# Optimization experiments

Hardware: AMD Instinct MI355X
Metric: run time of the kernel (lower is better)

Reference implementation:

```python
import jax, jax.numpy as jnp
import numpy as np

EPS = 1e-6
BN_EPS = 1e-5
K = 20

def vn_linear(x, W):
    # x: (B, Cin, 3, ...), W: (Cout, Cin)
    return jnp.einsum('oc,bc...->bo...', W, x)

def vn_batchnorm(x, gamma, beta):
    # x: (B, C, 3, ...). BN (training-mode batch stats) over per-channel vector norms.
    n = jnp.linalg.norm(x, axis=2) + EPS               # (B, C, ...)
    red = (0,) + tuple(range(2, n.ndim))
    mu = n.mean(red, keepdims=True)
    var = ((n - mu) ** 2).mean(red, keepdims=True)     # biased var, as BatchNorm uses
    sh = (1, -1) + (1,) * (n.ndim - 2)
    nbn = (n - mu) / jnp.sqrt(var + BN_EPS) * gamma.reshape(sh) + beta.reshape(sh)
    return x / n[:, :, None] * nbn[:, :, None]

def vn_leaky(x, Wf, Wd, gamma, beta, ns):
    # VNLinearLeakyReLU: linear -> VN batchnorm -> direction-gated leaky relu
    p = vn_batchnorm(vn_linear(x, Wf), gamma, beta)
    d = vn_linear(x, Wd)
    dot = jnp.sum(p * d, axis=2, keepdims=True)
    dsq = jnp.sum(d * d, axis=2, keepdims=True) + EPS
    neg = p - (dot / dsq) * d
    return ns * p + (1.0 - ns) * jnp.where(dot >= 0, p, neg)

def graph_feature_cross(x, k):
    # x: (B, N, 3) -> edge features (B, 3, 3, N, k): [nbr - x, x, nbr x x]
    sq = jnp.sum(x * x, axis=-1)                        # (B, N)
    d2 = sq[:, :, None] + sq[:, None, :] - 2.0 * jnp.einsum('bnd,bmd->bnm', x, x)
    idx = jax.lax.top_k(-d2, k)[1]                      # (B, N, k) nearest incl. self
    nbr = jax.vmap(lambda pts, ind: pts[ind])(x, idx)   # (B, N, k, 3)
    c = jnp.broadcast_to(x[:, :, None, :], nbr.shape)
    cr = jnp.cross(nbr, c)
    feat = jnp.stack([nbr - c, c, cr], axis=3)          # (B, N, k, 3ch, 3)
    return jnp.transpose(feat, (0, 3, 4, 1, 2))         # (B, 3, 3, N, k)


def setup_inputs() -> dict:
    key = jax.random.key(0)
    ks = iter(jax.random.split(key, 40))
    def W(shape):
        return jax.random.normal(next(ks), shape, jnp.float32) * 0.05
    d = {'x': jax.random.normal(next(ks), (2, 2048, 3), jnp.float32)}
    d.update(
        Wf_pos=W((21, 3)), Wd_pos=W((21, 3)), g_pos=jnp.ones(21), be_pos=jnp.zeros(21),
        Wf1=W((21, 21)), Wd1=W((21, 21)), g1=jnp.ones(21), be1=jnp.zeros(21),
        Wf2=W((42, 21)), Wd2=W((42, 21)), g2=jnp.ones(42), be2=jnp.zeros(42),
        W3=W((170, 42)), g3=jnp.ones(170), be3=jnp.zeros(170),
        Ws1f=W((170, 340)), Ws1d=W((170, 340)), gs1=jnp.ones(170), bs1=jnp.zeros(170),
        Ws2f=W((85, 170)), Ws2d=W((85, 170)), gs2=jnp.ones(85), bs2=jnp.zeros(85),
        Wstd=W((3, 85)),
        Wt1=W((1020, 1020)), Wt2=W((1020, 1020)), Wt3=W((14450, 1020)), bt3=jnp.zeros(14450),
    )
    return d


def reference(x, Wf_pos, Wd_pos, g_pos, be_pos, Wf1, Wd1, g1, be1, Wf2, Wd2, g2, be2,
              W3, g3, be3, Ws1f, Ws1d, gs1, bs1, Ws2f, Ws2d, gs2, bs2, Wstd,
              Wt1, Wt2, Wt3, bt3):
    B, N, _ = x.shape
    feat = graph_feature_cross(x, K)                                   # (B,3,3,N,K)
    h = vn_leaky(feat, Wf_pos, Wd_pos, g_pos, be_pos, 0.0).mean(-1)    # (B,21,3,N) pool over k
    h = vn_leaky(h, Wf1, Wd1, g1, be1, 0.0)                            # (B,21,3,N)
    h = vn_leaky(h, Wf2, Wd2, g2, be2, 0.0)                            # (B,42,3,N)
    h = vn_batchnorm(vn_linear(h, W3), g3, be3)                        # (B,170,3,N)
    z = h.mean(-1)                                                     # (B,170,3)
    h = jnp.concatenate([h, jnp.broadcast_to(z[..., None], z.shape + (N,))], axis=1)  # (B,340,3,N)
    # VNStdFeature (normalize_frame=False, default negative_slope=0.2 inside)
    z0 = vn_leaky(h, Ws1f, Ws1d, gs1, bs1, 0.2)                        # (B,170,3,N)
    z0 = vn_leaky(z0, Ws2f, Ws2d, gs2, bs2, 0.2)                       # (B,85,3,N)
    z0 = vn_linear(z0, Wstd)                                           # (B,3,3,N)
    hs = jnp.einsum('bijn,bjkn->bikn', h, z0)                          # (B,340,3,N) invariant feats
    t = hs.reshape(B, 340 * 3, N)                                      # (B,1020,N)
    t = jax.nn.relu(jnp.einsum('oc,bcn->bon', Wt1, t))
    t = jax.nn.relu(jnp.einsum('oc,bcn->bon', Wt2, t))
    t = jnp.einsum('oc,bcn->bon', Wt3, t) + bt3[None, :, None]         # (B,14450,N)
    theta = t.reshape(B, 85, 170, N)
    return (z, theta)
```

## Files before the change

### kernel.cpp

```cpp
#include <hip/hip_runtime.h>
#include <cstdint>
#include <cstddef>

constexpr int   BB     = 2;
constexpr int   NN     = 2048;
constexpr int   KNB    = 20;
constexpr float EPS_   = 1e-6f;
constexpr float BNEPS_ = 1e-5f;
constexpr int   KPAD   = 1024;
constexpr int   NTK    = KPAD / 64;
constexpr int   MT3    = 57;
constexpr int   MPAD3  = MT3 * 256;

typedef __bf16 bf16x8 __attribute__((ext_vector_type(8)));
typedef float  f32x4  __attribute__((ext_vector_type(4)));
typedef float  f32x2  __attribute__((ext_vector_type(2)));
typedef unsigned short u16x8 __attribute__((ext_vector_type(8)));

typedef const void t_gvoid __attribute__((address_space(1)));
typedef void       t_lvoid __attribute__((address_space(3)));

__device__ __forceinline__ unsigned short f2bf(float f) {
  unsigned int u = __builtin_bit_cast(unsigned int, f);
  u += 0x7FFFu + ((u >> 16) & 1u);
  return (unsigned short)(u >> 16);
}

__global__ __launch_bounds__(256) void knn_kernel(const float* __restrict__ x,
                                                  int* __restrict__ idx) {
  __shared__ float4 pts[NN];
  const int b = blockIdx.x >> 9;
  const int tid = threadIdx.x;
  const float* xb = x + (size_t)b * NN * 3;
  for (int i = tid; i < NN; i += 256) {
    float px = xb[i * 3], py = xb[i * 3 + 1], pz = xb[i * 3 + 2];
    pts[i] = make_float4(px, py, pz, px * px + py * py + pz * pz);
  }
  __syncthreads();
  const int wave = tid >> 6, lane = tid & 63;
  const int q = (blockIdx.x & 511) * 4 + wave;
  const float4 qp = pts[q];

  float d[32];
  #pragma unroll
  for (int i = 0; i < 32; ++i) {
    const float4 p = pts[lane + 64 * i];
    d[i] = qp.w + p.w - 2.0f * (qp.x * p.x + qp.y * p.y + qp.z * p.z);
  }

  float m; int mi;
  auto rescan = [&]() {
    m = 3.4e38f; mi = 0;
    #pragma unroll
    for (int i = 0; i < 32; ++i)
      if (d[i] < m) { m = d[i]; mi = i; }
  };
  rescan();

  int* op = idx + ((size_t)b * NN + q) * KNB;
  for (int r = 0; r < KNB; ++r) {
    float bm = m; int bj = lane + 64 * mi;
    #pragma unroll
    for (int s = 32; s > 0; s >>= 1) {
      const float om = __shfl_xor(bm, s, 64);
      const int   oj = __shfl_xor(bj, s, 64);
      if (om < bm || (om == bm && oj < bj)) { bm = om; bj = oj; }
    }
    if (lane == 0) op[r] = bj;
    if ((bj & 63) == lane) {
      const int ii = bj >> 6;
      #pragma unroll
      for (int i = 0; i < 32; ++i)
        if (i == ii) d[i] = 3.4e38f;
      rescan();
    }
  }
}

__global__ void feat_kernel(const float* __restrict__ x, const int* __restrict__ idx,
                            float* __restrict__ feat) {
  const int i = blockIdx.x * 256 + threadIdx.x;
  if (i >= BB * NN * KNB) return;
  const int n = (i / KNB) % NN, b = i / (KNB * NN);
  const float* xb = x + (size_t)b * NN * 3;
  const int j = idx[i];
  const float cx = xb[n * 3], cy = xb[n * 3 + 1], cz = xb[n * 3 + 2];
  const float nx = xb[j * 3], ny = xb[j * 3 + 1], nz = xb[j * 3 + 2];
  float* f = feat + (size_t)i * 9;
  f[0] = nx - cx; f[1] = ny - cy; f[2] = nz - cz;
  f[3] = cx;      f[4] = cy;      f[5] = cz;
  f[6] = ny * cz - nz * cy;
  f[7] = nz * cx - nx * cz;
  f[8] = nx * cy - ny * cx;
}

__global__ void l1_stats_part(const float* __restrict__ feat, const float* __restrict__ Wf,
                              float* __restrict__ part) {
  const int o = blockIdx.x, g = blockIdx.y, tid = threadIdx.x;
  const float w0 = Wf[o * 3], w1 = Wf[o * 3 + 1], w2 = Wf[o * 3 + 2];
  const int M = BB * NN * KNB;
  const int chunk = M / 8;
  float s1 = 0.f, s2 = 0.f;
  for (int i = g * chunk + tid; i < (g + 1) * chunk; i += 256) {
    const float* f = feat + (size_t)i * 9;
    float p0 = w0 * f[0] + w1 * f[3] + w2 * f[6];
    float p1 = w0 * f[1] + w1 * f[4] + w2 * f[7];
    float p2 = w0 * f[2] + w1 * f[5] + w2 * f[8];
    float nr = sqrtf(p0 * p0 + p1 * p1 + p2 * p2) + EPS_;
    s1 += nr; s2 += nr * nr;
  }
  __shared__ float rA[256], rB[256];
  rA[tid] = s1; rB[tid] = s2; __syncthreads();
  for (int off = 128; off > 0; off >>= 1) {
    if (tid < off) { rA[tid] += rA[tid + off]; rB[tid] += rB[tid + off]; }
    __syncthreads();
  }
  if (tid == 0) {
    part[(o * 8 + g) * 2]     = rA[0];
    part[(o * 8 + g) * 2 + 1] = rB[0];
  }
}

__global__ void l1_stats_fin(const float* __restrict__ part, const float* __restrict__ gamma,
                             float* __restrict__ stats) {
  const int o = threadIdx.x;
  if (o >= 21) return;
  const int M = BB * NN * KNB;
  float s1 = 0.f, s2 = 0.f;
  for (int g = 0; g < 8; ++g) { s1 += part[(o * 8 + g) * 2]; s2 += part[(o * 8 + g) * 2 + 1]; }
  float mu = s1 / M;
  float var = fmaxf(s2 / M - mu * mu, 0.f);
  stats[2 * o] = mu;
  stats[2 * o + 1] = gamma[o] / sqrtf(var + BNEPS_);
}

__global__ void l1_final_kernel(const float* __restrict__ feat, const float* __restrict__ Wf,
                                const float* __restrict__ Wd, const float* __restrict__ stats,
                                const float* __restrict__ beta, float* __restrict__ h1) {
  const int o = blockIdx.y, b = blockIdx.z;
  const int n = blockIdx.x * 256 + threadIdx.x;
  const float wf0 = Wf[o * 3], wf1 = Wf[o * 3 + 1], wf2 = Wf[o * 3 + 2];
  const float wd0 = Wd[o * 3], wd1 = Wd[o * 3 + 1], wd2 = Wd[o * 3 + 2];
  const float mu = stats[2 * o], sc = stats[2 * o + 1], be = beta[o];
  const float* fb = feat + ((size_t)(b * NN + n)) * KNB * 9;
  float a0 = 0.f, a1 = 0.f, a2 = 0.f;
  for (int k = 0; k < KNB; ++k) {
    const float* f = fb + k * 9;
    float p0 = wf0 * f[0] + wf1 * f[3] + wf2 * f[6];
    float p1 = wf0 * f[1] + wf1 * f[4] + wf2 * f[7];
    float p2 = wf0 * f[2] + wf1 * f[5] + wf2 * f[8];
    float d0 = wd0 * f[0] + wd1 * f[3] + wd2 * f[6];
    float d1 = wd0 * f[1] + wd1 * f[4] + wd2 * f[7];
    float d2 = wd0 * f[2] + wd1 * f[5] + wd2 * f[8];
    float nr = sqrtf(p0 * p0 + p1 * p1 + p2 * p2) + EPS_;
    float fac = ((nr - mu) * sc + be) / nr;
    p0 *= fac; p1 *= fac; p2 *= fac;
    float dot = p0 * d0 + p1 * d1 + p2 * d2;
    if (dot < 0.f) {
      float g = dot / (d0 * d0 + d1 * d1 + d2 * d2 + EPS_);
      p0 -= g * d0; p1 -= g * d1; p2 -= g * d2;
    }
    a0 += p0; a1 += p1; a2 += p2;
  }
  const size_t base = ((size_t)(b * 21 + o) * 3) * NN + n;
  h1[base]          = a0 * (1.f / KNB);
  h1[base + NN]     = a1 * (1.f / KNB);
  h1[base + 2 * NN] = a2 * (1.f / KNB);
}

__global__ void zbias_kernel(const float* __restrict__ zbuf, const float* __restrict__ Wf,
                             const float* __restrict__ Wd, float* __restrict__ zbf,
                             float* __restrict__ zbd, int Cout, int CinFull, int Cz) {
  const int bj = blockIdx.x;
  const int b = bj / 3, j = bj % 3;
  const int o = threadIdx.x;
  if (o >= Cout) return;
  const int off = CinFull - Cz;
  float sf = 0.f, sd = 0.f;
  for (int cz = 0; cz < Cz; ++cz) {
    const float zv = zbuf[((size_t)b * 170 + cz) * 3 + j];
    sf += Wf[(size_t)o * CinFull + off + cz] * zv;
    sd += Wd[(size_t)o * CinFull + off + cz] * zv;
  }
  zbf[(size_t)bj * Cout + o] = sf;
  zbd[(size_t)bj * Cout + o] = sd;
}

template <int HAS_D, int CONCAT_Z, int WRITE_STATS>
__global__ __launch_bounds__(256) void vn_lin_fused(
    const float* __restrict__ in, const float* __restrict__ Wf, const float* __restrict__ Wd,
    const float* __restrict__ zbf, const float* __restrict__ zbd,
    float* __restrict__ pout, float* __restrict__ dout, float* __restrict__ bpart,
    int Cin, int CinFull, int Cout) {
  __shared__ float wsh[(HAS_D ? 2 : 1) * 16 * 340];
  float* wfs = wsh;
  float* wds = HAS_D ? (wsh + 16 * 340) : wsh;
  const int tid = threadIdx.x;
  const int nt = blockIdx.x, ot = blockIdx.y, b = blockIdx.z;

  for (int i = tid; i < 16 * Cin; i += 256) {
    const int ol = i / Cin, c = i - ol * Cin;
    const int o = ot * 16 + ol;
    wfs[ol * Cin + c] = (o < Cout) ? Wf[(size_t)o * CinFull + c] : 0.f;
    if (HAS_D) wds[ol * Cin + c] = (o < Cout) ? Wd[(size_t)o * CinFull + c] : 0.f;
  }
  __syncthreads();

  const int lane = tid & 63, og = tid >> 6;
  const int n0 = nt * 128 + lane * 2;
  const float* ibase = in + ((size_t)b * Cin * 3) * NN + n0;

  f32x2 pf[4][3], pd[4][3];
  #pragma unroll
  for (int oo = 0; oo < 4; ++oo)
    #pragma unroll
    for (int j = 0; j < 3; ++j) {
      float bf = 0.f, bd = 0.f;
      if (CONCAT_Z) {
        const int o = ot * 16 + og * 4 + oo;
        if (o < Cout) {
          bf = zbf[(size_t)(b * 3 + j) * Cout + o];
          bd = zbd[(size_t)(b * 3 + j) * Cout + o];
        }
      }
      pf[oo][j] = (f32x2){bf, bf};
      pd[oo][j] = (f32x2){bd, bd};
    }

  #pragma unroll 2
  for (int c = 0; c < Cin; ++c) {
    f32x2 v[3];
    #pragma unroll
    for (int j = 0; j < 3; ++j)
      v[j] = *reinterpret_cast<const f32x2*>(ibase + ((size_t)c * 3 + j) * NN);
    #pragma unroll
    for (int oo = 0; oo < 4; ++oo) {
      const float wf = wfs[(og * 4 + oo) * Cin + c];
      #pragma unroll
      for (int j = 0; j < 3; ++j) pf[oo][j] += wf * v[j];
      if (HAS_D) {
        const float wd = wds[(og * 4 + oo) * Cin + c];
        #pragma unroll
        for (int j = 0; j < 3; ++j) pd[oo][j] += wd * v[j];
      }
    }
  }

  #pragma unroll
  for (int oo = 0; oo < 4; ++oo) {
    const int o = ot * 16 + og * 4 + oo;
    if (o < Cout) {
      const size_t ob = ((size_t)(b * Cout + o) * 3) * NN + n0;
      #pragma unroll
      for (int j = 0; j < 3; ++j) {
        *reinterpret_cast<f32x2*>(pout + ob + (size_t)j * NN) = pf[oo][j];
        if (HAS_D) *reinterpret_cast<f32x2*>(dout + ob + (size_t)j * NN) = pd[oo][j];
      }
    }
  }

  if (WRITE_STATS) {
    #pragma unroll
    for (int oo = 0; oo < 4; ++oo) {
      float s1 = 0.f, s2 = 0.f;
      #pragma unroll
      for (int t = 0; t < 2; ++t) {
        const float nr = sqrtf(pf[oo][0][t] * pf[oo][0][t] + pf[oo][1][t] * pf[oo][1][t] +
                               pf[oo][2][t] * pf[oo][2][t]) + EPS_;
        s1 += nr; s2 += nr * nr;
      }
      #pragma unroll
      for (int s = 32; s > 0; s >>= 1) {
        s1 += __shfl_xor(s1, s, 64);
        s2 += __shfl_xor(s2, s, 64);
      }
      const int o = ot * 16 + og * 4 + oo;
      if (lane == 0 && o < Cout) {
        bpart[(o * 32 + b * 16 + nt) * 2]     = s1;
        bpart[(o * 32 + b * 16 + nt) * 2 + 1] = s2;
      }
    }
  }
}

template <int GATE, int ZPART>
__global__ void vn_gate2(const float* __restrict__ p, const float* __restrict__ d,
                         const float* __restrict__ bpart, const float* __restrict__ gamma,
                         const float* __restrict__ beta, float* __restrict__ out,
                         float* __restrict__ zpart, int Cout, float ns) {
  const int o = blockIdx.y, b = blockIdx.z;
  const int n = blockIdx.x * 256 + threadIdx.x;
  const int M = BB * NN;
  float s1 = 0.f, s2 = 0.f;
  #pragma unroll 8
  for (int i = 0; i < 32; ++i) {
    s1 += bpart[(o * 32 + i) * 2];
    s2 += bpart[(o * 32 + i) * 2 + 1];
  }
  const float mu = s1 / M;
  const float var = fmaxf(s2 / M - mu * mu, 0.f);
  const float sc = gamma[o] / sqrtf(var + BNEPS_);
  const float be = beta[o];

  const size_t base = (((size_t)(b * Cout + o)) * 3) * NN + n;
  float p0 = p[base], p1 = p[base + NN], p2 = p[base + 2 * NN];
  const float nr = sqrtf(p0 * p0 + p1 * p1 + p2 * p2) + EPS_;
  const float fac = ((nr - mu) * sc + be) / nr;
  p0 *= fac; p1 *= fac; p2 *= fac;
  float o0 = p0, o1 = p1, o2 = p2;
  if (GATE) {
    const float d0 = d[base], d1 = d[base + NN], d2 = d[base + 2 * NN];
    const float dot = p0 * d0 + p1 * d1 + p2 * d2;
    if (dot < 0.f) {
      const float g = dot / (d0 * d0 + d1 * d1 + d2 * d2 + EPS_);
      o0 = p0 - g * d0; o1 = p1 - g * d1; o2 = p2 - g * d2;
    }
    o0 = ns * p0 + (1.f - ns) * o0;
    o1 = ns * p1 + (1.f - ns) * o1;
    o2 = ns * p2 + (1.f - ns) * o2;
  }
  out[base] = o0; out[base + NN] = o1; out[base + 2 * NN] = o2;

  if (ZPART) {
    float t0 = o0, t1 = o1, t2 = o2;
    #pragma unroll
    for (int s = 32; s > 0; s >>= 1) {
      t0 += __shfl_xor(t0, s, 64);
      t1 += __shfl_xor(t1, s, 64);
      t2 += __shfl_xor(t2, s, 64);
    }
    __shared__ float zsh[3][4];
    const int lane = threadIdx.x & 63, wv = threadIdx.x >> 6;
    if (lane == 0) { zsh[0][wv] = t0; zsh[1][wv] = t1; zsh[2][wv] = t2; }
    __syncthreads();
    if (threadIdx.x < 3) {
      const float s = zsh[threadIdx.x][0] + zsh[threadIdx.x][1] + zsh[threadIdx.x][2] + zsh[threadIdx.x][3];
      zpart[(size_t)(((b * Cout + o) * 3 + threadIdx.x)) * 8 + blockIdx.x] = s;
    }
  }
}

__global__ void zmean_fin(const float* __restrict__ zpart, float* __restrict__ zbuf,
                          float* __restrict__ outz) {
  const int idx = blockIdx.x * 256 + threadIdx.x;
  if (idx >= BB * 510) return;
  float s = 0.f;
  #pragma unroll
  for (int i = 0; i < 8; ++i) s += zpart[(size_t)idx * 8 + i];
  const float m = s / NN;
  zbuf[idx] = m;
  outz[idx] = m;
}

__global__ void hs_kernel(const float* __restrict__ h4, const float* __restrict__ zbuf,
                          const float* __restrict__ z0f, unsigned short* __restrict__ t0) {
  const int n = blockIdx.x;
  const int b = blockIdx.z;
  const int tid = threadIdx.x;
  __shared__ float zf[9];
  __shared__ float hcol[512];
  __shared__ float zcol[512];
  if (tid < 9) zf[tid] = z0f[(((size_t)(b * 3 + tid / 3)) * 3 + (tid % 3)) * NN + n];
  for (int i = tid; i < 510; i += 256) {
    hcol[i] = h4[((size_t)b * 510 + i) * NN + n];
    zcol[i] = zbuf[(size_t)b * 510 + i];
  }
  __syncthreads();
  unsigned short* trow = t0 + ((size_t)b * NN + n) * KPAD;
  for (int c = tid; c < KPAD; c += 256) {
    if (c >= 1020) { trow[c] = 0; continue; }
    const int i = c / 3, kv = c % 3;
    float acc = 0.f;
    #pragma unroll
    for (int j = 0; j < 3; ++j) {
      const float hv = (i < 170) ? hcol[i * 3 + j] : zcol[(i - 170) * 3 + j];
      acc += hv * zf[j * 3 + kv];
    }
    trow[c] = f2bf(acc);
  }
}

__global__ void wconv_kernel(const float* __restrict__ W, unsigned short* __restrict__ out,
                             int M, int Kv, size_t total8) {
  size_t i = (size_t)blockIdx.x * 256 + threadIdx.x;
  const size_t stride = (size_t)gridDim.x * 256;
  for (; i < total8; i += stride) {
    const size_t e = i * 8;
    const int k = (int)(e & (KPAD - 1));
    const int o = (int)(e >> 10);
    u16x8 v;
    if (o < M && k + 8 <= Kv) {
      const float* src = W + (size_t)o * Kv + k;
      #pragma unroll
      for (int t = 0; t < 8; ++t) v[t] = f2bf(src[t]);
    } else {
      #pragma unroll
      for (int t = 0; t < 8; ++t) {
        const int kk = k + t;
        v[t] = (o < M && kk < Kv) ? f2bf(W[(size_t)o * Kv + kk]) : (unsigned short)0;
      }
    }
    *reinterpret_cast<u16x8*>(out + e) = v;
  }
}

template <int RELU>
__global__ __launch_bounds__(256) void gemm_kernel(
    const unsigned short* __restrict__ A, const unsigned short* __restrict__ Bmat,
    unsigned short* __restrict__ outB, int M) {
  __shared__ __align__(16) unsigned short lA[2][128 * 64];
  __shared__ __align__(16) unsigned short lB[2][128 * 64];
  const int tid = threadIdx.x;
  const int nwg = gridDim.x, q = nwg >> 3;
  const int orig = blockIdx.x;
  const int swz = (orig & 7) * q + (orig >> 3);
  const int ntile = swz & 15;
  const int mtile = (swz >> 4) & 7;
  const int b = swz >> 7;
  const int lane = tid & 63, w = tid >> 6;
  const int wm = w >> 1, wn = w & 1;
  const int lrow = lane & 15, lgrp = lane >> 4;

  const unsigned short* Abase = A + (size_t)mtile * 128 * KPAD;
  const unsigned short* Bbase = Bmat + ((size_t)b * NN + (size_t)ntile * 128) * KPAD;

  const int rowS = tid >> 3;
  const int scol = ((tid & 7) * 8) ^ ((rowS & 7) * 8);
  const int wb8  = __builtin_amdgcn_readfirstlane(tid & 192) * 8;

  f32x4 acc[4][4];
  #pragma unroll
  for (int mi = 0; mi < 4; ++mi)
    #pragma unroll
    for (int ni = 0; ni < 4; ++ni) acc[mi][ni] = (f32x4){0.f, 0.f, 0.f, 0.f};

  auto stage = [&](int bufi, int kt) {
    const int kof = kt * 64;
    #pragma unroll
    for (int r = 0; r < 4; ++r) {
      __builtin_amdgcn_global_load_lds(
          (t_gvoid*)(Abase + (size_t)(r * 32 + rowS) * KPAD + kof + scol),
          (t_lvoid*)&lA[bufi][r * 2048 + wb8], 16, 0, 0);
      __builtin_amdgcn_global_load_lds(
          (t_gvoid*)(Bbase + (size_t)(r * 32 + rowS) * KPAD + kof + scol),
          (t_lvoid*)&lB[bufi][r * 2048 + wb8], 16, 0, 0);
    }
  };

  stage(0, 0);
  for (int kt = 0; kt < NTK; ++kt) {
    const int cur = kt & 1;
    if (kt + 1 < NTK) {
      stage(cur ^ 1, kt + 1);
      asm volatile("s_waitcnt vmcnt(8)" ::: "memory");
    } else {
      asm volatile("s_waitcnt vmcnt(0)" ::: "memory");
    }
    asm volatile("s_barrier" ::: "memory");

    bf16x8 af[4][2], bfr[4][2];
    #pragma unroll
    for (int mi = 0; mi < 4; ++mi) {
      const int ra = wm * 64 + mi * 16 + lrow;
      const int rb = wn * 64 + mi * 16 + lrow;
      #pragma unroll
      for (int kk = 0; kk < 2; ++kk) {
        af[mi][kk]  = *reinterpret_cast<const bf16x8*>(
            &lA[cur][ra * 64 + ((kk * 32 + lgrp * 8) ^ ((ra & 7) * 8))]);
        bfr[mi][kk] = *reinterpret_cast<const bf16x8*>(
            &lB[cur][rb * 64 + ((kk * 32 + lgrp * 8) ^ ((rb & 7) * 8))]);
      }
    }
    #pragma unroll
    for (int kk = 0; kk < 2; ++kk)
      #pragma unroll
      for (int mi = 0; mi < 4; ++mi)
        #pragma unroll
        for (int ni = 0; ni < 4; ++ni)
          acc[mi][ni] = __builtin_amdgcn_mfma_f32_16x16x32_bf16(af[mi][kk], bfr[ni][kk],
                                                                acc[mi][ni], 0, 0, 0);
    asm volatile("s_barrier" ::: "memory");
  }

  const int fr_col = lane & 15;
  const int fr_rowb = (lane >> 4) * 4;
  #pragma unroll
  for (int mi = 0; mi < 4; ++mi) {
    const int rowb = mtile * 128 + wm * 64 + mi * 16 + fr_rowb;
    #pragma unroll
    for (int ni = 0; ni < 4; ++ni) {
      const int col = ntile * 128 + wn * 64 + ni * 16 + fr_col;
      ushort4 v;
      if (rowb < M) {
        float u0 = acc[mi][ni][0], u1 = acc[mi][ni][1], u2 = acc[mi][ni][2], u3 = acc[mi][ni][3];
        if (RELU) { u0 = fmaxf(u0, 0.f); u1 = fmaxf(u1, 0.f); u2 = fmaxf(u2, 0.f); u3 = fmaxf(u3, 0.f); }
        v.x = f2bf(u0); v.y = f2bf(u1); v.z = f2bf(u2); v.w = f2bf(u3);
      } else {
        v.x = v.y = v.z = v.w = 0;
      }
      *reinterpret_cast<ushort4*>(outB + ((size_t)b * NN + col) * KPAD + rowb) = v;
    }
  }
}

__global__ __launch_bounds__(512, 2) void gemm256_kernel(
    const unsigned short* __restrict__ A, const unsigned short* __restrict__ Bmat,
    float* __restrict__ outF, const float* __restrict__ bias, int M, int MT) {
  __shared__ __align__(16) unsigned short lA[2][256 * 64];
  __shared__ __align__(16) unsigned short lB[2][256 * 64];
  const int tid = threadIdx.x;
  const int nwg = gridDim.x, q = nwg >> 3;
  const int orig = blockIdx.x;
  const int swz = (orig & 7) * q + (orig >> 3);
  const int ntile = swz & 7;
  const int rem = swz >> 3;
  const int mtile = rem % MT;
  const int b = rem / MT;
  const int lane = tid & 63, w = tid >> 6;
  const int wm = w >> 2, wn = w & 3;
  const int lrow = lane & 15, lgrp = lane >> 4;

  const unsigned short* Abase = A + (size_t)mtile * 256 * KPAD;
  const unsigned short* Bbase = Bmat + ((size_t)b * NN + (size_t)ntile * 256) * KPAD;

  const int rowS = tid >> 3;
  const int scol = ((tid & 7) * 8) ^ ((rowS & 7) * 8);
  const int wb8  = __builtin_amdgcn_readfirstlane((tid & 448) >> 6) * 512;

  f32x4 acc[8][4];
  #pragma unroll
  for (int mi = 0; mi < 8; ++mi)
    #pragma unroll
    for (int ni = 0; ni < 4; ++ni) acc[mi][ni] = (f32x4){0.f, 0.f, 0.f, 0.f};

  auto stage = [&](int bufi, int kt) {
    const int kof = kt * 64;
    #pragma unroll
    for (int r = 0; r < 4; ++r) {
      __builtin_amdgcn_global_load_lds(
          (t_gvoid*)(Abase + (size_t)(r * 64 + rowS) * KPAD + kof + scol),
          (t_lvoid*)&lA[bufi][r * 4096 + wb8], 16, 0, 0);
      __builtin_amdgcn_global_load_lds(
          (t_gvoid*)(Bbase + (size_t)(r * 64 + rowS) * KPAD + kof + scol),
          (t_lvoid*)&lB[bufi][r * 4096 + wb8], 16, 0, 0);
    }
  };

  stage(0, 0);
  for (int kt = 0; kt < NTK; ++kt) {
    const int cur = kt & 1;
    if (kt + 1 < NTK) {
      stage(cur ^ 1, kt + 1);
      asm volatile("s_waitcnt vmcnt(8)" ::: "memory");
    } else {
      asm volatile("s_waitcnt vmcnt(0)" ::: "memory");
    }
    asm volatile("s_barrier" ::: "memory");

    #pragma unroll
    for (int kk = 0; kk < 2; ++kk) {
      bf16x8 af[8], bfr[4];
      #pragma unroll
      for (int mi = 0; mi < 8; ++mi) {
        const int ra = wm * 128 + mi * 16 + lrow;
        af[mi] = *reinterpret_cast<const bf16x8*>(
            &lA[cur][ra * 64 + ((kk * 32 + lgrp * 8) ^ ((ra & 7) * 8))]);
      }
      #pragma unroll
      for (int ni = 0; ni < 4; ++ni) {
        const int rb = wn * 64 + ni * 16 + lrow;
        bfr[ni] = *reinterpret_cast<const bf16x8*>(
            &lB[cur][rb * 64 + ((kk * 32 + lgrp * 8) ^ ((rb & 7) * 8))]);
      }
      #pragma unroll
      for (int mi = 0; mi < 8; ++mi)
        #pragma unroll
        for (int ni = 0; ni < 4; ++ni)
          acc[mi][ni] = __builtin_amdgcn_mfma_f32_16x16x32_bf16(af[mi], bfr[ni],
                                                                acc[mi][ni], 0, 0, 0);
    }
    asm volatile("s_barrier" ::: "memory");
  }

  const int fr_col = lane & 15;
  const int fr_rowb = (lane >> 4) * 4;
  #pragma unroll
  for (int mi = 0; mi < 8; ++mi) {
    const int rowb = mtile * 256 + wm * 128 + mi * 16 + fr_rowb;
    #pragma unroll
    for (int ni = 0; ni < 4; ++ni) {
      const int col = ntile * 256 + wn * 64 + ni * 16 + fr_col;
      #pragma unroll
      for (int r = 0; r < 4; ++r) {
        const int rr = rowb + r;
        if (rr < M) outF[((size_t)b * M + rr) * NN + col] = acc[mi][ni][r] + bias[rr];
      }
    }
  }
}

extern "C" void kernel_launch(void* const* d_in, const int* in_sizes, int n_in,
                              void* d_out, int out_size, void* d_ws, size_t ws_size,
                              hipStream_t stream) {
  const float* x      = (const float*)d_in[0];
  const float* Wf_pos = (const float*)d_in[1];
  const float* Wd_pos = (const float*)d_in[2];
  const float* g_pos  = (const float*)d_in[3];
  const float* be_pos = (const float*)d_in[4];
  const float* Wf1    = (const float*)d_in[5];
  const float* Wd1    = (const float*)d_in[6];
  const float* g1     = (const float*)d_in[7];
  const float* be1    = (const float*)d_in[8];
  const float* Wf2    = (const float*)d_in[9];
  const float* Wd2    = (const float*)d_in[10];
  const float* g2     = (const float*)d_in[11];
  const float* be2    = (const float*)d_in[12];
  const float* W3     = (const float*)d_in[13];
  const float* g3     = (const float*)d_in[14];
  const float* be3    = (const float*)d_in[15];
  const float* Ws1f   = (const float*)d_in[16];
  const float* Ws1d   = (const float*)d_in[17];
  const float* gs1    = (const float*)d_in[18];
  const float* bs1    = (const float*)d_in[19];
  const float* Ws2f   = (const float*)d_in[20];
  const float* Ws2d   = (const float*)d_in[21];
  const float* gs2    = (const float*)d_in[22];
  const float* bs2    = (const float*)d_in[23];
  const float* Wstd   = (const float*)d_in[24];
  const float* Wt1    = (const float*)d_in[25];
  const float* Wt2    = (const float*)d_in[26];
  const float* Wt3    = (const float*)d_in[27];
  const float* bt3    = (const float*)d_in[28];
  (void)in_sizes; (void)n_in; (void)out_size; (void)ws_size;

  float* out = (float*)d_out;
  float* out_theta = out + 1020;

  char* ws = (char*)d_ws;
  size_t off = 0;
  auto alloc = [&](size_t bytes) -> void* {
    void* p = (void*)(ws + off);
    off += (bytes + 255) & ~(size_t)255;
    return p;
  };
  int*            idx  = (int*)           alloc((size_t)BB * NN * KNB * 4);
  float*          feat = (float*)         alloc((size_t)BB * NN * KNB * 9 * 4);
  float*          stats= (float*)         alloc(1024 * 4);
  float*          part = (float*)         alloc(2048 * 4);
  float*          bpart= (float*)         alloc((size_t)170 * 32 * 2 * 4);
  float*          zpart= (float*)         alloc((size_t)510 * BB * 8 * 4);
  float*          h1   = (float*)         alloc((size_t)BB * 21 * 3 * NN * 4);
  float*          h2   = (float*)         alloc((size_t)BB * 21 * 3 * NN * 4);
  float*          h3   = (float*)         alloc((size_t)BB * 42 * 3 * NN * 4);
  float*          h4   = (float*)         alloc((size_t)BB * 170 * 3 * NN * 4);
  float*          zbuf = (float*)         alloc((size_t)BB * 170 * 3 * 4);
  float*          pbuf = (float*)         alloc((size_t)BB * 170 * 3 * NN * 4);
  float*          dbuf = (float*)         alloc((size_t)BB * 170 * 3 * NN * 4);
  float*          z0a  = (float*)         alloc((size_t)BB * 170 * 3 * NN * 4);
  float*          z0b  = (float*)         alloc((size_t)BB * 85 * 3 * NN * 4);
  float*          z0f  = (float*)         alloc((size_t)BB * 3 * 3 * NN * 4);
  float*          zbf  = (float*)         alloc((size_t)6 * 170 * 4);
  float*          zbd  = (float*)         alloc((size_t)6 * 170 * 4);
  unsigned short* W1b  = (unsigned short*)alloc((size_t)1024 * KPAD * 2);
  unsigned short* W2b  = (unsigned short*)alloc((size_t)1024 * KPAD * 2);
  unsigned short* W3b  = (unsigned short*)alloc((size_t)MPAD3 * KPAD * 2);
  unsigned short* t0   = (unsigned short*)alloc((size_t)BB * NN * KPAD * 2);
  unsigned short* t1   = (unsigned short*)alloc((size_t)BB * NN * KPAD * 2);
  unsigned short* t2   = t0;

  knn_kernel<<<BB * 512, 256, 0, stream>>>(x, idx);
  feat_kernel<<<(BB * NN * KNB + 255) / 256, 256, 0, stream>>>(x, idx, feat);
  l1_stats_part<<<dim3(21, 8), 256, 0, stream>>>(feat, Wf_pos, part);
  l1_stats_fin<<<1, 64, 0, stream>>>(part, g_pos, stats);
  l1_final_kernel<<<dim3(8, 21, BB), 256, 0, stream>>>(feat, Wf_pos, Wd_pos, stats, be_pos, h1);

  vn_lin_fused<1, 0, 1><<<dim3(16, 2, BB), 256, 0, stream>>>(h1, Wf1, Wd1, nullptr, nullptr, pbuf, dbuf, bpart, 21, 21, 21);
  vn_gate2<1, 0><<<dim3(8, 21, BB), 256, 0, stream>>>(pbuf, dbuf, bpart, g1, be1, h2, nullptr, 21, 0.0f);

  vn_lin_fused<1, 0, 1><<<dim3(16, 3, BB), 256, 0, stream>>>(h2, Wf2, Wd2, nullptr, nullptr, pbuf, dbuf, bpart, 21, 21, 42);
  vn_gate2<1, 0><<<dim3(8, 42, BB), 256, 0, stream>>>(pbuf, dbuf, bpart, g2, be2, h3, nullptr, 42, 0.0f);

  vn_lin_fused<0, 0, 1><<<dim3(16, 11, BB), 256, 0, stream>>>(h3, W3, nullptr, nullptr, nullptr, pbuf, nullptr, bpart, 42, 42, 170);
  vn_gate2<0, 1><<<dim3(8, 170, BB), 256, 0, stream>>>(pbuf, nullptr, bpart, g3, be3, h4, zpart, 170, 0.0f);

  zmean_fin<<<(BB * 510 + 255) / 256, 256, 0, stream>>>(zpart, zbuf, out);

  zbias_kernel<<<6, 256, 0, stream>>>(zbuf, Ws1f, Ws1d, zbf, zbd, 170, 340, 170);
  vn_lin_fused<1, 1, 1><<<dim3(16, 11, BB), 256, 0, stream>>>(h4, Ws1f, Ws1d, zbf, zbd, pbuf, dbuf, bpart, 170, 340, 170);
  vn_gate2<1, 0><<<dim3(8, 170, BB), 256, 0, stream>>>(pbuf, dbuf, bpart, gs1, bs1, z0a, nullptr, 170, 0.2f);

  vn_lin_fused<1, 0, 1><<<dim3(16, 6, BB), 256, 0, stream>>>(z0a, Ws2f, Ws2d, nullptr, nullptr, pbuf, dbuf, bpart, 170, 170, 85);
  vn_gate2<1, 0><<<dim3(8, 85, BB), 256, 0, stream>>>(pbuf, dbuf, bpart, gs2, bs2, z0b, nullptr, 85, 0.2f);

  vn_lin_fused<0, 0, 0><<<dim3(16, 1, BB), 256, 0, stream>>>(z0b, Wstd, nullptr, nullptr, nullptr, z0f, nullptr, nullptr, 85, 85, 3);

  hs_kernel<<<dim3(NN, 1, BB), 256, 0, stream>>>(h4, zbuf, z0f, t0);

  wconv_kernel<<<512, 256, 0, stream>>>(Wt1, W1b, 1020, 1020, (size_t)1024 * KPAD / 8);
  wconv_kernel<<<512, 256, 0, stream>>>(Wt2, W2b, 1020, 1020, (size_t)1024 * KPAD / 8);
  wconv_kernel<<<2048, 256, 0, stream>>>(Wt3, W3b, 14450, 1020, (size_t)MPAD3 * KPAD / 8);

  gemm_kernel<1><<<256, 256, 0, stream>>>(W1b, t0, t1, 1020);
  gemm_kernel<1><<<256, 256, 0, stream>>>(W2b, t1, t2, 1020);
  gemm256_kernel<<<8 * MT3 * BB, 512, 0, stream>>>(W3b, t2, out_theta, bt3, 14450, MT3);
}
```

Before: 586.2 us.

## Widen VN linear to four points per thread and tile hs kernel over points

The VN linear kernel now processes four points per thread with 128-bit loads and stores. That halves the grid and the number of batch-stat partials, and the gate kernel's reduction is shrunk to match. The hs kernel is retiled so each block handles 16 points, staging the h4 columns in padded shared memory. This replaces the old one-point-per-block launch, whose column reads were strided and uncoalesced. The trade-off is fewer blocks, which lowers occupancy on the small linear layers, and higher register pressure.

Measured after the change: 677.0 us, median of 2. 1.15x slower.

```diff
diff --git a/kernel.cpp b/kernel.cpp
--- a/kernel.cpp
+++ b/kernel.cpp
@@ -11,10 +11,10 @@
 constexpr int   NTK    = KPAD / 64;
 constexpr int   MT3    = 57;
 constexpr int   MPAD3  = MT3 * 256;
+constexpr int   HST    = 16;
 
 typedef __bf16 bf16x8 __attribute__((ext_vector_type(8)));
 typedef float  f32x4  __attribute__((ext_vector_type(4)));
-typedef float  f32x2  __attribute__((ext_vector_type(2)));
 typedef unsigned short u16x8 __attribute__((ext_vector_type(8)));
 
 typedef const void t_gvoid __attribute__((address_space(1)));
@@ -187,7 +187,7 @@
 }
 
 template <int HAS_D, int CONCAT_Z, int WRITE_STATS>
-__global__ __launch_bounds__(256) void vn_lin_fused(
+__global__ __launch_bounds__(256) void vn_lin_fused4(
     const float* __restrict__ in, const float* __restrict__ Wf, const float* __restrict__ Wd,
     const float* __restrict__ zbf, const float* __restrict__ zbd,
     float* __restrict__ pout, float* __restrict__ dout, float* __restrict__ bpart,
@@ -207,10 +207,10 @@
   __syncthreads();
 
   const int lane = tid & 63, og = tid >> 6;
-  const int n0 = nt * 128 + lane * 2;
+  const int n0 = nt * 256 + lane * 4;
   const float* ibase = in + ((size_t)b * Cin * 3) * NN + n0;
 
-  f32x2 pf[4][3], pd[4][3];
+  f32x4 pf[4][3], pd[4][3];
   #pragma unroll
   for (int oo = 0; oo < 4; ++oo)
     #pragma unroll
@@ -223,16 +223,16 @@
           bd = zbd[(size_t)(b * 3 + j) * Cout + o];
         }
       }
-      pf[oo][j] = (f32x2){bf, bf};
-      pd[oo][j] = (f32x2){bd, bd};
+      pf[oo][j] = (f32x4){bf, bf, bf, bf};
+      pd[oo][j] = (f32x4){bd, bd, bd, bd};
     }
 
   #pragma unroll 2
   for (int c = 0; c < Cin; ++c) {
-    f32x2 v[3];
+    f32x4 v[3];
     #pragma unroll
     for (int j = 0; j < 3; ++j)
-      v[j] = *reinterpret_cast<const f32x2*>(ibase + ((size_t)c * 3 + j) * NN);
+      v[j] = *reinterpret_cast<const f32x4*>(ibase + ((size_t)c * 3 + j) * NN);
     #pragma unroll
     for (int oo = 0; oo < 4; ++oo) {
       const float wf = wfs[(og * 4 + oo) * Cin + c];
@@ -253,8 +253,8 @@
       const size_t ob = ((size_t)(b * Cout + o) * 3) * NN + n0;
       #pragma unroll
       for (int j = 0; j < 3; ++j) {
-        *reinterpret_cast<f32x2*>(pout + ob + (size_t)j * NN) = pf[oo][j];
-        if (HAS_D) *reinterpret_cast<f32x2*>(dout + ob + (size_t)j * NN) = pd[oo][j];
+        *reinterpret_cast<f32x4*>(pout + ob + (size_t)j * NN) = pf[oo][j];
+        if (HAS_D) *reinterpret_cast<f32x4*>(dout + ob + (size_t)j * NN) = pd[oo][j];
       }
     }
   }
@@ -264,7 +264,7 @@
     for (int oo = 0; oo < 4; ++oo) {
       float s1 = 0.f, s2 = 0.f;
       #pragma unroll
-      for (int t = 0; t < 2; ++t) {
+      for (int t = 0; t < 4; ++t) {
         const float nr = sqrtf(pf[oo][0][t] * pf[oo][0][t] + pf[oo][1][t] * pf[oo][1][t] +
                                pf[oo][2][t] * pf[oo][2][t]) + EPS_;
         s1 += nr; s2 += nr * nr;
@@ -276,8 +276,8 @@
       }
       const int o = ot * 16 + og * 4 + oo;
       if (lane == 0 && o < Cout) {
-        bpart[(o * 32 + b * 16 + nt) * 2]     = s1;
-        bpart[(o * 32 + b * 16 + nt) * 2 + 1] = s2;
+        bpart[(o * 16 + b * 8 + nt) * 2]     = s1;
+        bpart[(o * 16 + b * 8 + nt) * 2 + 1] = s2;
       }
     }
   }
@@ -292,10 +292,10 @@
   const int n = blockIdx.x * 256 + threadIdx.x;
   const int M = BB * NN;
   float s1 = 0.f, s2 = 0.f;
-  #pragma unroll 8
-  for (int i = 0; i < 32; ++i) {
-    s1 += bpart[(o * 32 + i) * 2];
-    s2 += bpart[(o * 32 + i) * 2 + 1];
+  #pragma unroll
+  for (int i = 0; i < 16; ++i) {
+    s1 += bpart[(o * 16 + i) * 2];
+    s2 += bpart[(o * 16 + i) * 2 + 1];
   }
   const float mu = s1 / M;
   const float var = fmaxf(s2 / M - mu * mu, 0.f);
@@ -352,31 +352,46 @@
   outz[idx] = m;
 }
 
-__global__ void hs_kernel(const float* __restrict__ h4, const float* __restrict__ zbuf,
-                          const float* __restrict__ z0f, unsigned short* __restrict__ t0) {
-  const int n = blockIdx.x;
+__global__ __launch_bounds__(256) void hs_kernel(const float* __restrict__ h4,
+                                                 const float* __restrict__ zbuf,
+                                                 const float* __restrict__ z0f,
+                                                 unsigned short* __restrict__ t0) {
+  const int n0 = blockIdx.x * HST;
   const int b = blockIdx.z;
   const int tid = threadIdx.x;
-  __shared__ float zf[9];
-  __shared__ float hcol[512];
-  __shared__ float zcol[512];
-  if (tid < 9) zf[tid] = z0f[(((size_t)(b * 3 + tid / 3)) * 3 + (tid % 3)) * NN + n];
-  for (int i = tid; i < 510; i += 256) {
-    hcol[i] = h4[((size_t)b * 510 + i) * NN + n];
-    zcol[i] = zbuf[(size_t)b * 510 + i];
+  __shared__ float hcol[510 * (HST + 1)];
+  __shared__ float zcol[510];
+  __shared__ float zf[9 * HST];
+  for (int i = tid; i < 510; i += 256) zcol[i] = zbuf[(size_t)b * 510 + i];
+  if (tid < 9 * HST) {
+    const int jk = tid / HST, nl = tid % HST;
+    zf[jk * HST + nl] = z0f[((size_t)(b * 9) + jk) * NN + n0 + nl];
+  }
+  const int nl = tid & (HST - 1);
+  for (int i = tid / HST; i < 510; i += 256 / HST) {
+    hcol[i * (HST + 1) + nl] = h4[((size_t)b * 510 + i) * NN + n0 + nl];
   }
   __syncthreads();
-  unsigned short* trow = t0 + ((size_t)b * NN + n) * KPAD;
-  for (int c = tid; c < KPAD; c += 256) {
-    if (c >= 1020) { trow[c] = 0; continue; }
-    const int i = c / 3, kv = c % 3;
-    float acc = 0.f;
-    #pragma unroll
-    for (int j = 0; j < 3; ++j) {
-      const float hv = (i < 170) ? hcol[i * 3 + j] : zcol[(i - 170) * 3 + j];
-      acc += hv * zf[j * 3 + kv];
-    }
-    trow[c] = f2bf(acc);
+
+  const int lane = tid & 63, w = tid >> 6;
+  unsigned short* tbase = t0 + ((size_t)b * NN + n0) * KPAD;
+  for (int nn = 0; nn < HST / 4; ++nn) {
+    const int nc = w * (HST / 4) + nn;
+    unsigned short* trow = tbase + (size_t)nc * KPAD;
+    for (int cc = 0; cc < KPAD / 64; ++cc) {
+      const int c = cc * 64 + lane;
+      float acc = 0.f;
+      if (c < 1020) {
+        const int i = c / 3, kv = c - i * 3;
+        #pragma unroll
+        for (int j = 0; j < 3; ++j) {
+          const float hv = (i < 170) ? hcol[(i * 3 + j) * (HST + 1) + nc]
+                                     : zcol[(i - 170) * 3 + j];
+          acc += hv * zf[(j * 3 + kv) * HST + nc];
+        }
+      }
+      trow[c] = f2bf(acc);
+    }
   }
 }
 
@@ -647,7 +662,7 @@
   float*          feat = (float*)         alloc((size_t)BB * NN * KNB * 9 * 4);
   float*          stats= (float*)         alloc(1024 * 4);
   float*          part = (float*)         alloc(2048 * 4);
-  float*          bpart= (float*)         alloc((size_t)170 * 32 * 2 * 4);
+  float*          bpart= (float*)         alloc((size_t)170 * 16 * 2 * 4);
   float*          zpart= (float*)         alloc((size_t)510 * BB * 8 * 4);
   float*          h1   = (float*)         alloc((size_t)BB * 21 * 3 * NN * 4);
   float*          h2   = (float*)         alloc((size_t)BB * 21 * 3 * NN * 4);
@@ -674,27 +689,27 @@
   l1_stats_fin<<<1, 64, 0, stream>>>(part, g_pos, stats);
   l1_final_kernel<<<dim3(8, 21, BB), 256, 0, stream>>>(feat, Wf_pos, Wd_pos, stats, be_pos, h1);
 
-  vn_lin_fused<1, 0, 1><<<dim3(16, 2, BB), 256, 0, stream>>>(h1, Wf1, Wd1, nullptr, nullptr, pbuf, dbuf, bpart, 21, 21, 21);
+  vn_lin_fused4<1, 0, 1><<<dim3(8, 2, BB), 256, 0, stream>>>(h1, Wf1, Wd1, nullptr, nullptr, pbuf, dbuf, bpart, 21, 21, 21);
   vn_gate2<1, 0><<<dim3(8, 21, BB), 256, 0, stream>>>(pbuf, dbuf, bpart, g1, be1, h2, nullptr, 21, 0.0f);
 
-  vn_lin_fused<1, 0, 1><<<dim3(16, 3, BB), 256, 0, stream>>>(h2, Wf2, Wd2, nullptr, nullptr, pbuf, dbuf, bpart, 21, 21, 42);
+  vn_lin_fused4<1, 0, 1><<<dim3(8, 3, BB), 256, 0, stream>>>(h2, Wf2, Wd2, nullptr, nullptr, pbuf, dbuf, bpart, 21, 21, 42);
   vn_gate2<1, 0><<<dim3(8, 42, BB), 256, 0, stream>>>(pbuf, dbuf, bpart, g2, be2, h3, nullptr, 42, 0.0f);
 
-  vn_lin_fused<0, 0, 1><<<dim3(16, 11, BB), 256, 0, stream>>>(h3, W3, nullptr, nullptr, nullptr, pbuf, nullptr, bpart, 42, 42, 170);
+  vn_lin_fused4<0, 0, 1><<<dim3(8, 11, BB), 256, 0, stream>>>(h3, W3, nullptr, nullptr, nullptr, pbuf, nullptr, bpart, 42, 42, 170);
   vn_gate2<0, 1><<<dim3(8, 170, BB), 256, 0, stream>>>(pbuf, nullptr, bpart, g3, be3, h4, zpart, 170, 0.0f);
 
   zmean_fin<<<(BB * 510 + 255) / 256, 256, 0, stream>>>(zpart, zbuf, out);
 
   zbias_kernel<<<6, 256, 0, stream>>>(zbuf, Ws1f, Ws1d, zbf, zbd, 170, 340, 170);
-  vn_lin_fused<1, 1, 1><<<dim3(16, 11, BB), 256, 0, stream>>>(h4, Ws1f, Ws1d, zbf, zbd, pbuf, dbuf, bpart, 170, 340, 170);
+  vn_lin_fused4<1, 1, 1><<<dim3(8, 11, BB), 256, 0, stream>>>(h4, Ws1f, Ws1d, zbf, zbd, pbuf, dbuf, bpart, 170, 340, 170);
   vn_gate2<1, 0><<<dim3(8, 170, BB), 256, 0, stream>>>(pbuf, dbuf, bpart, gs1, bs1, z0a, nullptr, 170, 0.2f);
 
-  vn_lin_fused<1, 0, 1><<<dim3(16, 6, BB), 256, 0, stream>>>(z0a, Ws2f, Ws2d, nullptr, nullptr, pbuf, dbuf, bpart, 170, 170, 85);
+  vn_lin_fused4<1, 0, 1><<<dim3(8, 6, BB), 256, 0, stream>>>(z0a, Ws2f, Ws2d, nullptr, nullptr, pbuf, dbuf, bpart, 170, 170, 85);
   vn_gate2<1, 0><<<dim3(8, 85, BB), 256, 0, stream>>>(pbuf, dbuf, bpart, gs2, bs2, z0b, nullptr, 85, 0.2f);
 
-  vn_lin_fused<0, 0, 0><<<dim3(16, 1, BB), 256, 0, stream>>>(z0b, Wstd, nullptr, nullptr, nullptr, z0f, nullptr, nullptr, 85, 85, 3);
-
-  hs_kernel<<<dim3(NN, 1, BB), 256, 0, stream>>>(h4, zbuf, z0f, t0);
+  vn_lin_fused4<0, 0, 0><<<dim3(8, 1, BB), 256, 0, stream>>>(z0b, Wstd, nullptr, nullptr, nullptr, z0f, nullptr, nullptr, 85, 85, 3);
+
+  hs_kernel<<<dim3(NN / HST, 1, BB), 256, 0, stream>>>(h4, zbuf, z0f, t0);
 
   wconv_kernel<<<512, 256, 0, stream>>>(Wt1, W1b, 1020, 1020, (size_t)1024 * KPAD / 8);
   wconv_kernel<<<512, 256, 0, stream>>>(Wt2, W2b, 1020, 1020, (size_t)1024 * KPAD / 8);
```
